# Performance work log

Hardware: AMD Instinct MI355X
Metric: run time of the kernel (lower is better)

The kernel has to match this reference:

```python
import jax, jax.numpy as jnp
import numpy as np

N = 50000      # nodes
E = 800000     # edges (before self loops)
G = 256        # graphs in batch
N_IN, NHID, HEADS, NOUT = 128, 64, 2, 768
ATT_SLOPE = 0.2   # GATv2 attention LeakyReLU slope (PyG default)
ACT_SLOPE = 0.01  # nn.LeakyReLU default slope


def setup_inputs() -> dict:
    key = jax.random.key(0)
    ks = jax.random.split(key, 20)
    def lin_w(k, fo, fi):
        return (jax.random.normal(k, (fo, fi), jnp.float32) / np.sqrt(fi)).astype(jnp.float32)
    x = jax.random.normal(ks[0], (N, N_IN), jnp.float32)
    edge_index = jax.random.randint(ks[1], (2, E), 0, N, dtype=jnp.int64)
    batch = jnp.sort(jax.random.randint(ks[2], (N,), 0, G, dtype=jnp.int64))
    HC = HEADS * NHID
    return {
        "x": x, "edge_index": edge_index, "batch": batch,
        # conv1: GATv2Conv(N_IN -> NHID, heads=HEADS)
        "w1_l": lin_w(ks[3], HC, N_IN), "b1_l": jnp.zeros((HC,), jnp.float32),
        "w1_r": lin_w(ks[4], HC, N_IN), "b1_r": jnp.zeros((HC,), jnp.float32),
        "att1": jax.random.normal(ks[5], (HEADS, NHID), jnp.float32) / np.sqrt(NHID),
        "bias1": jnp.zeros((HC,), jnp.float32),
        # conv2: GATv2Conv(HC -> NHID, heads=1)
        "w2_l": lin_w(ks[6], NHID, HC), "b2_l": jnp.zeros((NHID,), jnp.float32),
        "w2_r": lin_w(ks[7], NHID, HC), "b2_r": jnp.zeros((NHID,), jnp.float32),
        "att2": jax.random.normal(ks[8], (1, NHID), jnp.float32) / np.sqrt(NHID),
        "bias2": jnp.zeros((NHID,), jnp.float32),
        # MLP head
        "fc1_w": lin_w(ks[9], NHID, NHID), "fc1_b": jnp.zeros((NHID,), jnp.float32),
        "fc2_w": lin_w(ks[10], NOUT, NHID), "fc2_b": jnp.zeros((NOUT,), jnp.float32),
    }


def _leaky(v, slope):
    return jnp.where(v > 0, v, slope * v)


def gatv2_conv(x, src, dst, w_l, b_l, w_r, b_r, att, bias, heads, ch):
    n = x.shape[0]
    xl = (x @ w_l.T + b_l).reshape(n, heads, ch)   # source transform
    xr = (x @ w_r.T + b_r).reshape(n, heads, ch)   # target transform
    m = _leaky(xl[src] + xr[dst], ATT_SLOPE)       # [E, H, C]
    e = jnp.einsum('ehc,hc->eh', m, att)           # attention logits
    # segment softmax over incoming edges of each dst node (self loops guarantee non-empty)
    emax = jax.ops.segment_max(e, dst, num_segments=n)
    ex = jnp.exp(e - emax[dst])
    denom = jax.ops.segment_sum(ex, dst, num_segments=n)
    alpha = ex / denom[dst]
    out = jax.ops.segment_sum(xl[src] * alpha[:, :, None], dst, num_segments=n)
    return out.reshape(n, heads * ch) + bias


def reference(x, edge_index, batch, w1_l, b1_l, w1_r, b1_r, att1, bias1,
              w2_l, b2_l, w2_r, b2_r, att2, bias2, fc1_w, fc1_b, fc2_w, fc2_b):
    loops = jnp.arange(N, dtype=edge_index.dtype)
    src = jnp.concatenate([edge_index[0], loops])  # PyG adds self loops by default
    dst = jnp.concatenate([edge_index[1], loops])
    h = gatv2_conv(x, src, dst, w1_l, b1_l, w1_r, b1_r, att1, bias1, HEADS, NHID)
    h = _leaky(h, ACT_SLOPE)
    h = gatv2_conv(h, src, dst, w2_l, b2_l, w2_r, b2_r, att2, bias2, 1, NHID)
    h = _leaky(h, ACT_SLOPE)
    # global mean pool over graphs
    sums = jax.ops.segment_sum(h, batch, num_segments=G)
    cnt = jax.ops.segment_sum(jnp.ones((N,), h.dtype), batch, num_segments=G)
    pooled = sums / jnp.maximum(cnt, 1.0)[:, None]
    h = _leaky(pooled @ fc1_w.T + fc1_b, ACT_SLOPE)
    return h @ fc2_w.T + fc2_b
```

## Files before the change

### kernel.cpp

```cpp
#include <hip/hip_runtime.h>

#define ATT_SLOPE 0.2f
#define ACT_SLOPE 0.01f

typedef _Float16 half8  __attribute__((ext_vector_type(8)));
typedef _Float16 half2v __attribute__((ext_vector_type(2)));
typedef float    floatx4 __attribute__((ext_vector_type(4)));

#if defined(__has_builtin)
#if __has_builtin(__builtin_amdgcn_fdot2)
#define HAVE_FDOT2 1
#endif
#endif

__device__ __forceinline__ float lrelu(float v, float s) {
    return fmaxf(v, v * s);
}

__device__ __forceinline__ half2v lrelu2(half2v m) {
    half2v t = m * (_Float16)ATT_SLOPE;
    return __builtin_elementwise_max(m, t);
}

__device__ __forceinline__ float dot2(half2v a, half2v b, float c) {
#ifdef HAVE_FDOT2
    return __builtin_amdgcn_fdot2(a, b, c, false);
#else
    return c + (float)a[0] * (float)b[0] + (float)a[1] * (float)b[1];
#endif
}


__global__ __launch_bounds__(256) void k_count_rank(const int* __restrict__ ei, int E, int N,
                                                    int* __restrict__ deg,
                                                    int* __restrict__ rank) {
    int i = blockIdx.x * 256 + threadIdx.x;
    int total = E + N;
    if (i >= total) return;
    int dst = (i < E) ? ei[E + i] : (i - E);
    rank[i] = atomicAdd(&deg[dst], 1);
}

__global__ __launch_bounds__(256) void k_scan_block(const int* __restrict__ deg, int n,
                                                    int* __restrict__ rp1, int* __restrict__ bsum) {
    __shared__ int s[256];
    int tid = threadIdx.x;
    int i = blockIdx.x * 256 + tid;
    s[tid] = (i < n) ? deg[i] : 0;
    __syncthreads();
    for (int off = 1; off < 256; off <<= 1) {
        int t = (tid >= off) ? s[tid - off] : 0;
        __syncthreads();
        s[tid] += t;
        __syncthreads();
    }
    if (i < n) rp1[i] = s[tid];
    if (tid == 255) bsum[blockIdx.x] = s[255];
}

__global__ __launch_bounds__(256) void k_scan_add(int* __restrict__ rowptr,
                                                  const int* __restrict__ bsum, int n) {
    __shared__ int s[256];
    int tid = threadIdx.x, bid = blockIdx.x;
    s[tid] = (tid < bid) ? bsum[tid] : 0;
    __syncthreads();
    for (int off = 128; off > 0; off >>= 1) {
        if (tid < off) s[tid] += s[tid + off];
        __syncthreads();
    }
    int boff = s[0];
    int i = bid * 256 + tid;
    if (i < n) rowptr[i + 1] += boff;
    if (i == 0) rowptr[0] = 0;
}


__global__ __launch_bounds__(256) void k_encode_w(const float* __restrict__ w1l,
                                                  const float* __restrict__ w1r,
                                                  const float* __restrict__ w2l,
                                                  const float* __restrict__ w2r,
                                                  _Float16* __restrict__ W1h,
                                                  _Float16* __restrict__ W1lo,
                                                  _Float16* __restrict__ W2h,
                                                  _Float16* __restrict__ W2lo,
                                                  float* __restrict__ gsum, int gn,
                                                  int* __restrict__ deg, int n) {
    int i = blockIdx.x * 256 + threadIdx.x;
    if (i >= 49152 + gn + n) return;
    if (i >= 49152 + gn) {
        deg[i - 49152 - gn] = 0;
        return;
    }
    if (i >= 49152) {
        gsum[i - 49152] = 0.f;
        return;
    }
    float v;
    _Float16 *ph, *pl;
    int idx;
    if (i < 32768) {
        idx = i;
        v = (i < 16384) ? w1l[i] : w1r[i - 16384];
        ph = W1h; pl = W1lo;
    } else {
        int j = i - 32768;
        idx = j;
        v = (j < 8192) ? w2l[j] : w2r[j - 8192];
        ph = W2h; pl = W2lo;
    }
    _Float16 h = (_Float16)v;
    ph[idx] = h;
    pl[idx] = (_Float16)(v - (float)h);
}


template <int COUT, bool IN_F32>
__device__ __forceinline__ void gemm_body(int bid, int tid,
                                          _Float16 (*sWh)[40], _Float16 (*sWl)[40],
                                          const float* __restrict__ Af,
                                          const _Float16* __restrict__ Ahi,
                                          const _Float16* __restrict__ Alo, int n_rows,
                                          const _Float16* __restrict__ Whi,
                                          const _Float16* __restrict__ Wlo,
                                          const float* __restrict__ B0,
                                          const float* __restrict__ B1,
                                          _Float16* __restrict__ out) {
    constexpr int NT = COUT / 16;
    const int lane = tid & 63, wv = tid >> 6;
    const int m = lane & 15, q = lane >> 4;
    const long row0 = ((long)bid * 4 + wv) * 16;
    const bool active = row0 < n_rows;
    const long arow = row0 + m;

    floatx4 acc[NT] = {};
    for (int kk = 0; kk < 128; kk += 32) {
        __syncthreads();
        for (int t = tid; t < COUT * 4; t += 256) {
            int c = t >> 2, ch = t & 3;
            *(half8*)&sWh[c][ch * 8] = *(const half8*)&Whi[(size_t)c * 128 + kk + ch * 8];
            *(half8*)&sWl[c][ch * 8] = *(const half8*)&Wlo[(size_t)c * 128 + kk + ch * 8];
        }
        __syncthreads();
        if (active) {
            half8 ah, al;
            if constexpr (IN_F32) {
                float4 a0 = *(const float4*)&Af[(size_t)arow * 128 + kk + q * 8];
                float4 a1 = *(const float4*)&Af[(size_t)arow * 128 + kk + q * 8 + 4];
                float av[8] = {a0.x, a0.y, a0.z, a0.w, a1.x, a1.y, a1.z, a1.w};
                #pragma unroll
                for (int x = 0; x < 8; ++x) {
                    ah[x] = (_Float16)av[x];
                    al[x] = (_Float16)(av[x] - (float)ah[x]);
                }
            } else {
                ah = *(const half8*)&Ahi[(size_t)arow * 128 + kk + q * 8];
                al = *(const half8*)&Alo[(size_t)arow * 128 + kk + q * 8];
            }
            #pragma unroll
            for (int nt = 0; nt < NT; ++nt) {
                half8 bh = *(const half8*)&sWh[nt * 16 + m][q * 8];
                half8 bl = *(const half8*)&sWl[nt * 16 + m][q * 8];
                acc[nt] = __builtin_amdgcn_mfma_f32_16x16x32_f16(ah, bh, acc[nt], 0, 0, 0);
                acc[nt] = __builtin_amdgcn_mfma_f32_16x16x32_f16(al, bh, acc[nt], 0, 0, 0);
                acc[nt] = __builtin_amdgcn_mfma_f32_16x16x32_f16(ah, bl, acc[nt], 0, 0, 0);
            }
        }
    }
    if (active) {
        #pragma unroll
        for (int nt = 0; nt < NT; ++nt) {
            int col = nt * 16 + m;
            float b = (col < COUT / 2) ? B0[col] : B1[col - COUT / 2];
            #pragma unroll
            for (int r = 0; r < 4; ++r) {
                long grow = row0 + q * 4 + r;
                out[(size_t)grow * COUT + col] = (_Float16)(acc[nt][r] + b);
            }
        }
    }
}

__global__ __launch_bounds__(256) void k_gemm1_scatter(const float* __restrict__ x,
                                                       const _Float16* __restrict__ W1h,
                                                       const _Float16* __restrict__ W1lo,
                                                       const float* __restrict__ B0,
                                                       const float* __restrict__ B1,
                                                       _Float16* __restrict__ buf1, int n_rows,
                                                       const int* __restrict__ ei, int E,
                                                       const int* __restrict__ rowptr,
                                                       const int* __restrict__ rank,
                                                       int* __restrict__ adj, int gB) {
    __shared__ _Float16 sWh[256][40];
    __shared__ _Float16 sWl[256][40];
    const int bid = blockIdx.x, tid = threadIdx.x;
    if (bid < gB) {
        gemm_body<256, true>(bid, tid, sWh, sWl, x, nullptr, nullptr, n_rows,
                             W1h, W1lo, B0, B1, buf1);
    } else {
        int i = (bid - gB) * 256 + tid;
        int T = E + n_rows;
        if (i < T) {
            int dst = (i < E) ? ei[E + i] : (i - E);
            int src = (i < E) ? ei[i] : dst;
            adj[rowptr[dst] + rank[i]] = src;
        }
    }
}

template <int COUT, bool IN_F32>
__global__ __launch_bounds__(256) void gemm_mfma(const float* __restrict__ Af,
                                                 const _Float16* __restrict__ Ahi,
                                                 const _Float16* __restrict__ Alo, int n_rows,
                                                 const _Float16* __restrict__ Whi,
                                                 const _Float16* __restrict__ Wlo,
                                                 const float* __restrict__ B0,
                                                 const float* __restrict__ B1,
                                                 _Float16* __restrict__ out) {
    __shared__ _Float16 sWh[COUT][40];
    __shared__ _Float16 sWl[COUT][40];
    gemm_body<COUT, IN_F32>(blockIdx.x, threadIdx.x, sWh, sWl, Af, Ahi, Alo, n_rows,
                            Whi, Wlo, B0, B1, out);
}


__global__ __launch_bounds__(128) void conv1_fused(const _Float16* __restrict__ buf,
                                                   const int* __restrict__ rowptr,
                                                   const int* __restrict__ adj,
                                                   const float* __restrict__ att,
                                                   const float* __restrict__ bias,
                                                   _Float16* __restrict__ h1hi,
                                                   _Float16* __restrict__ h1lo, int n) {
    __shared__ _Float16 sxl[2][16][136];
    __shared__ _Float16 sxr[2][128];
    __shared__ float    sw[2][2][16];
    __shared__ _Float16 satt[128];
    const int tid = threadIdx.x, lane = tid & 63, wv = tid >> 6;
    satt[tid] = (_Float16)att[tid];
    __syncthreads();
    int node = blockIdx.x * 2 + wv;
    if (node >= n) return;

    const int jlane = lane & 15;
    const int grp = lane >> 4;
    const int chq = grp * 32;
    const int head = grp >> 1;
    const int wselg = lane >> 5;
    if (lane < 16)
        *(half8*)&sxr[wv][lane * 8] = *(const half8*)&buf[(size_t)node * 256 + 128 + lane * 8];
    asm volatile("s_waitcnt lgkmcnt(0)" ::: "memory");

    const int s = rowptr[node], e = rowptr[node + 1];
    float2 accA = {0.f, 0.f}, accB = {0.f, 0.f};
    float denA = 0.f, denB = 0.f;
    for (int c0 = s; c0 < e; c0 += 16) {
        const int cnt = min(16, e - c0);
        float sacc0 = 0.f, sacc1 = 0.f;
        if (jlane < cnt) {
            int src = adj[c0 + jlane];
            const _Float16* xlp = &buf[(size_t)src * 256 + chq];
            #pragma unroll
            for (int k = 0; k < 4; ++k) {
                half8 l = *(const half8*)&xlp[k * 8];
                half8 r = *(const half8*)&sxr[wv][chq + k * 8];
                half8 a = *(const half8*)&satt[chq + k * 8];
                *(half8*)&sxl[wv][jlane][chq + k * 8] = l;
                float* sp = (k & 1) ? &sacc1 : &sacc0;
                #pragma unroll
                for (int p = 0; p < 4; ++p) {
                    half2v lp = {l[2 * p], l[2 * p + 1]};
                    half2v rp = {r[2 * p], r[2 * p + 1]};
                    half2v ap = {a[2 * p], a[2 * p + 1]};
                    *sp = dot2(lrelu2(lp + rp), ap, *sp);
                }
            }
        }
        float sacc = sacc0 + sacc1;
        float efull = sacc + __shfl_xor(sacc, 16);
        if ((grp & 1) == 0 && jlane < cnt) sw[wv][head][jlane] = __expf(efull);
        asm volatile("s_waitcnt lgkmcnt(0)" ::: "memory");
        int j = 0;
        for (; j + 1 < cnt; j += 2) {
            float w0 = sw[wv][wselg][j], w1 = sw[wv][wselg][j + 1];
            half2v v0 = *(const half2v*)&sxl[wv][j][lane * 2];
            half2v v1 = *(const half2v*)&sxl[wv][j + 1][lane * 2];
            accA.x += w0 * (float)v0[0]; accA.y += w0 * (float)v0[1]; denA += w0;
            accB.x += w1 * (float)v1[0]; accB.y += w1 * (float)v1[1]; denB += w1;
        }
        if (j < cnt) {
            float w0 = sw[wv][wselg][j];
            half2v v0 = *(const half2v*)&sxl[wv][j][lane * 2];
            accA.x += w0 * (float)v0[0]; accA.y += w0 * (float)v0[1]; denA += w0;
        }
        asm volatile("s_waitcnt lgkmcnt(0)" ::: "memory");
    }
    float inv = 1.f / (denA + denB);
    float2 b = *(const float2*)&bias[lane * 2];
    float ox = lrelu((accA.x + accB.x) * inv + b.x, ACT_SLOPE);
    float oy = lrelu((accA.y + accB.y) * inv + b.y, ACT_SLOPE);
    half2v hv, lv;
    hv[0] = (_Float16)ox; lv[0] = (_Float16)(ox - (float)hv[0]);
    hv[1] = (_Float16)oy; lv[1] = (_Float16)(oy - (float)hv[1]);
    *(half2v*)&h1hi[(size_t)node * 128 + lane * 2] = hv;
    *(half2v*)&h1lo[(size_t)node * 128 + lane * 2] = lv;
}


__global__ __launch_bounds__(128) void conv2_fused(const _Float16* __restrict__ buf,
                                                   const int* __restrict__ rowptr,
                                                   const int* __restrict__ adj,
                                                   const float* __restrict__ att,
                                                   const float* __restrict__ bias,
                                                   const int* __restrict__ batch,
                                                   float* __restrict__ gsum, int n) {
    __shared__ _Float16 sxl[2][32][72];
    __shared__ _Float16 sxr[2][64];
    __shared__ float    sw[2][32];
    __shared__ _Float16 satt[64];
    const int tid = threadIdx.x, lane = tid & 63, wv = tid >> 6;
    if (tid < 64) satt[tid] = (_Float16)att[tid];
    __syncthreads();
    int node = blockIdx.x * 2 + wv;
    if (node >= n) return;

    const int j = lane & 31;
    const int g = lane >> 5;
    const int ch0 = g * 32;
    if (lane < 8)
        *(half8*)&sxr[wv][lane * 8] = *(const half8*)&buf[(size_t)node * 128 + 64 + lane * 8];
    asm volatile("s_waitcnt lgkmcnt(0)" ::: "memory");

    const int s = rowptr[node], e = rowptr[node + 1];
    float accA = 0.f, accB = 0.f, denA = 0.f, denB = 0.f;
    for (int c0 = s; c0 < e; c0 += 32) {
        const int cnt = min(32, e - c0);
        float sacc = 0.f;
        if (j < cnt) {
            int src = adj[c0 + j];
            const _Float16* xlp = &buf[(size_t)src * 128 + ch0];
            #pragma unroll
            for (int k = 0; k < 4; ++k) {
                half8 l = *(const half8*)&xlp[k * 8];
                half8 r = *(const half8*)&sxr[wv][ch0 + k * 8];
                half8 a = *(const half8*)&satt[ch0 + k * 8];
                *(half8*)&sxl[wv][j][ch0 + k * 8] = l;
                #pragma unroll
                for (int p = 0; p < 4; ++p) {
                    half2v lp = {l[2 * p], l[2 * p + 1]};
                    half2v rp = {r[2 * p], r[2 * p + 1]};
                    half2v ap = {a[2 * p], a[2 * p + 1]};
                    sacc = dot2(lrelu2(lp + rp), ap, sacc);
                }
            }
        }
        float efull = sacc + __shfl_xor(sacc, 32);
        if (g == 0 && j < cnt) sw[wv][j] = __expf(efull);
        asm volatile("s_waitcnt lgkmcnt(0)" ::: "memory");
        int jj = 0;
        for (; jj + 1 < cnt; jj += 2) {
            float w0 = sw[wv][jj], w1 = sw[wv][jj + 1];
            accA += w0 * (float)sxl[wv][jj][lane];     denA += w0;
            accB += w1 * (float)sxl[wv][jj + 1][lane]; denB += w1;
        }
        if (jj < cnt) {
            float w0 = sw[wv][jj];
            accA += w0 * (float)sxl[wv][jj][lane];
            denA += w0;
        }
        asm volatile("s_waitcnt lgkmcnt(0)" ::: "memory");
    }
    float val = lrelu((accA + accB) / (denA + denB) + bias[lane], ACT_SLOPE);
    atomicAdd(&gsum[(size_t)batch[node] * 64 + lane], val);
}


__device__ __forceinline__ int lower_bound(const int* a, int n, int v) {
    int lo = 0, hi = n;
    while (lo < hi) { int mid = (lo + hi) >> 1; if (a[mid] < v) lo = mid + 1; else hi = mid; }
    return lo;
}

__global__ __launch_bounds__(256) void pool_mlp(const float* __restrict__ gsum,
                                                const int* __restrict__ batch,
                                                const float* __restrict__ fc1_w,
                                                const float* __restrict__ fc1_b,
                                                const float* __restrict__ fc2_w,
                                                const float* __restrict__ fc2_b,
                                                float* __restrict__ out, int n) {
    const int g = blockIdx.x;
    const int tid = threadIdx.x;
    __shared__ float pooled[64];
    __shared__ float hmid[64];

    int lo = lower_bound(batch, n, g);
    int hi = lower_bound(batch, n, g + 1);
    float inv = 1.f / (float)max(hi - lo, 1);

    if (tid < 64) pooled[tid] = gsum[(size_t)g * 64 + tid] * inv;
    __syncthreads();
    if (tid < 64) {
        float acc = fc1_b[tid];
        const float* w = &fc1_w[(size_t)tid * 64];
        #pragma unroll
        for (int k = 0; k < 64; ++k) acc += pooled[k] * w[k];
        hmid[tid] = lrelu(acc, ACT_SLOPE);
    }
    __syncthreads();
    for (int o = tid; o < 768; o += 256) {
        float acc = fc2_b[o];
        const float* w = &fc2_w[(size_t)o * 64];
        #pragma unroll
        for (int k = 0; k < 64; ++k) acc += hmid[k] * w[k];
        out[(size_t)g * 768 + o] = acc;
    }
}


extern "C" void kernel_launch(void* const* d_in, const int* in_sizes, int n_in,
                              void* d_out, int out_size, void* d_ws, size_t ws_size,
                              hipStream_t stream) {
    const float* x     = (const float*)d_in[0];
    const int*   ei    = (const int*)d_in[1];
    const int*   batch = (const int*)d_in[2];
    const float* w1_l  = (const float*)d_in[3];
    const float* b1_l  = (const float*)d_in[4];
    const float* w1_r  = (const float*)d_in[5];
    const float* b1_r  = (const float*)d_in[6];
    const float* att1  = (const float*)d_in[7];
    const float* bias1 = (const float*)d_in[8];
    const float* w2_l  = (const float*)d_in[9];
    const float* b2_l  = (const float*)d_in[10];
    const float* w2_r  = (const float*)d_in[11];
    const float* b2_r  = (const float*)d_in[12];
    const float* att2  = (const float*)d_in[13];
    const float* bias2 = (const float*)d_in[14];
    const float* fc1_w = (const float*)d_in[15];
    const float* fc1_b = (const float*)d_in[16];
    const float* fc2_w = (const float*)d_in[17];
    const float* fc2_b = (const float*)d_in[18];
    float* out = (float*)d_out;

    const int N = in_sizes[2];
    const int E = in_sizes[1] / 2;
    const int T = E + N;
    const int G = out_size / 768;

    char* ws = (char*)d_ws;
    size_t off = 0;
    auto alloc = [&](size_t bytes) -> void* {
        void* p = ws + off;
        off = (off + bytes + 255) & ~(size_t)255;
        return p;
    };
    int*      deg    = (int*)alloc((size_t)N * 4);
    int*      rowptr = (int*)alloc((size_t)(N + 1) * 4);
    int*      rank   = (int*)alloc((size_t)T * 4);
    int*      bsum   = (int*)alloc(1024);
    int*      adj    = (int*)alloc((size_t)T * 4);
    _Float16* h1hi   = (_Float16*)alloc((size_t)N * 128 * 2);
    _Float16* h1lo   = (_Float16*)alloc((size_t)N * 128 * 2);
    _Float16* W1h    = (_Float16*)alloc(32768 * 2);
    _Float16* W1lo   = (_Float16*)alloc(32768 * 2);
    _Float16* W2h    = (_Float16*)alloc(16384 * 2);
    _Float16* W2lo   = (_Float16*)alloc(16384 * 2);
    float*    gsum   = (float*)alloc((size_t)G * 64 * 4);
    _Float16* buf1   = (_Float16*)alloc((size_t)N * 256 * 2);
    _Float16* buf2 = buf1;

    const int nbN  = (N + 255) / 256;
    const int nbT  = (T + 255) / 256;
    const int mfmG = (N / 16 + 3) / 4;
    const int edgG = (N + 1) / 2;
    const int encG = (49152 + G * 64 + N + 255) / 256;

    k_encode_w<<<encG, 256, 0, stream>>>(w1_l, w1_r, w2_l, w2_r,
                                         W1h, W1lo, W2h, W2lo, gsum, G * 64, deg, N);

    k_count_rank<<<nbT, 256, 0, stream>>>(ei, E, N, deg, rank);
    k_scan_block<<<nbN, 256, 0, stream>>>(deg, N, rowptr + 1, bsum);
    k_scan_add<<<nbN, 256, 0, stream>>>(rowptr, bsum, N);

    k_gemm1_scatter<<<mfmG + nbT, 256, 0, stream>>>(x, W1h, W1lo, b1_l, b1_r, buf1, N,
                                                    ei, E, rowptr, rank, adj, mfmG);

    conv1_fused<<<edgG, 128, 0, stream>>>(buf1, rowptr, adj, att1, bias1, h1hi, h1lo, N);

    gemm_mfma<128, false><<<mfmG, 256, 0, stream>>>(nullptr, h1hi, h1lo, N,
                                                    W2h, W2lo, b2_l, b2_r, buf2);
    conv2_fused<<<edgG, 128, 0, stream>>>(buf2, rowptr, adj, att2, bias2, batch, gsum, N);

    pool_mlp<<<G, 256, 0, stream>>>(gsum, batch, fc1_w, fc1_b, fc2_w, fc2_b, out, N);
}
```

Measured before the change: 298.0 us.

## Process nodes in descending-degree order via counting-sort permutation for load balance

Adds a degree histogram in the scan kernel and a new counting-sort kernel that builds a permutation of nodes ordered by descending in-degree (capped at 63). Both conv kernels now process nodes in that order, so high-degree nodes are scheduled first and similar-degree nodes share a block. This targets tail imbalance and divergence between the two waves of a block. It costs an extra kernel launch and an indirection. Output writes become scattered and lose coalescing, and the conv2 batch-pooling atomics lose their locality.

Measured after the change: 291.6 us, median of 2. -2.2%, faster.

```diff
diff --git a/kernel.cpp b/kernel.cpp
--- a/kernel.cpp
+++ b/kernel.cpp
@@ -42,12 +42,17 @@
 }
 
 __global__ __launch_bounds__(256) void k_scan_block(const int* __restrict__ deg, int n,
-                                                    int* __restrict__ rp1, int* __restrict__ bsum) {
+                                                    int* __restrict__ rp1, int* __restrict__ bsum,
+                                                    int* __restrict__ hist) {
     __shared__ int s[256];
+    __shared__ int lh[64];
     int tid = threadIdx.x;
     int i = blockIdx.x * 256 + tid;
-    s[tid] = (i < n) ? deg[i] : 0;
-    __syncthreads();
+    int dv = (i < n) ? deg[i] : 0;
+    s[tid] = dv;
+    if (tid < 64) lh[tid] = 0;
+    __syncthreads();
+    if (i < n) atomicAdd(&lh[min(dv, 63)], 1);
     for (int off = 1; off < 256; off <<= 1) {
         int t = (tid >= off) ? s[tid - off] : 0;
         __syncthreads();
@@ -56,6 +61,7 @@
     }
     if (i < n) rp1[i] = s[tid];
     if (tid == 255) bsum[blockIdx.x] = s[255];
+    if (tid < 64 && lh[tid]) atomicAdd(&hist[tid], lh[tid]);
 }
 
 __global__ __launch_bounds__(256) void k_scan_add(int* __restrict__ rowptr,
@@ -72,6 +78,27 @@
     int i = bid * 256 + tid;
     if (i < n) rowptr[i + 1] += boff;
     if (i == 0) rowptr[0] = 0;
+}
+
+__global__ __launch_bounds__(256) void k_perm(const int* __restrict__ deg, int n,
+                                              const int* __restrict__ hist,
+                                              int* __restrict__ cursor,
+                                              int* __restrict__ perm) {
+    __shared__ int lh[64], gb[64], bb[64];
+    int tid = threadIdx.x, i = blockIdx.x * 256 + tid;
+    if (tid < 64) lh[tid] = 0;
+    __syncthreads();
+    int b = 0, lpos = 0;
+    if (i < n) { b = min(deg[i], 63); lpos = atomicAdd(&lh[b], 1); }
+    __syncthreads();
+    if (tid < 64) {
+        gb[tid] = lh[tid] ? atomicAdd(&cursor[tid], lh[tid]) : 0;
+        int s = 0;
+        for (int k = 63; k > tid; --k) s += hist[k];
+        bb[tid] = s;
+    }
+    __syncthreads();
+    if (i < n) perm[bb[b] + gb[b] + lpos] = i;
 }
 
 
@@ -84,9 +111,14 @@
                                                   _Float16* __restrict__ W2h,
                                                   _Float16* __restrict__ W2lo,
                                                   float* __restrict__ gsum, int gn,
-                                                  int* __restrict__ deg, int n) {
+                                                  int* __restrict__ deg, int n,
+                                                  int* __restrict__ hc) {
     int i = blockIdx.x * 256 + threadIdx.x;
-    if (i >= 49152 + gn + n) return;
+    if (i >= 49152 + gn + n + 128) return;
+    if (i >= 49152 + gn + n) {
+        hc[i - 49152 - gn - n] = 0;
+        return;
+    }
     if (i >= 49152 + gn) {
         deg[i - 49152 - gn] = 0;
         return;
@@ -226,6 +258,7 @@
 __global__ __launch_bounds__(128) void conv1_fused(const _Float16* __restrict__ buf,
                                                    const int* __restrict__ rowptr,
                                                    const int* __restrict__ adj,
+                                                   const int* __restrict__ perm,
                                                    const float* __restrict__ att,
                                                    const float* __restrict__ bias,
                                                    _Float16* __restrict__ h1hi,
@@ -237,8 +270,9 @@
     const int tid = threadIdx.x, lane = tid & 63, wv = tid >> 6;
     satt[tid] = (_Float16)att[tid];
     __syncthreads();
-    int node = blockIdx.x * 2 + wv;
-    if (node >= n) return;
+    int idx = blockIdx.x * 2 + wv;
+    if (idx >= n) return;
+    int node = perm[idx];
 
     const int jlane = lane & 15;
     const int grp = lane >> 4;
@@ -308,6 +342,7 @@
 __global__ __launch_bounds__(128) void conv2_fused(const _Float16* __restrict__ buf,
                                                    const int* __restrict__ rowptr,
                                                    const int* __restrict__ adj,
+                                                   const int* __restrict__ perm,
                                                    const float* __restrict__ att,
                                                    const float* __restrict__ bias,
                                                    const int* __restrict__ batch,
@@ -319,8 +354,9 @@
     const int tid = threadIdx.x, lane = tid & 63, wv = tid >> 6;
     if (tid < 64) satt[tid] = (_Float16)att[tid];
     __syncthreads();
-    int node = blockIdx.x * 2 + wv;
-    if (node >= n) return;
+    int idx = blockIdx.x * 2 + wv;
+    if (idx >= n) return;
+    int node = perm[idx];
 
     const int j = lane & 31;
     const int g = lane >> 5;
@@ -455,6 +491,8 @@
     int*      rowptr = (int*)alloc((size_t)(N + 1) * 4);
     int*      rank   = (int*)alloc((size_t)T * 4);
     int*      bsum   = (int*)alloc(1024);
+    int*      hc     = (int*)alloc(128 * 4);
+    int*      perm   = (int*)alloc((size_t)N * 4);
     int*      adj    = (int*)alloc((size_t)T * 4);
     _Float16* h1hi   = (_Float16*)alloc((size_t)N * 128 * 2);
     _Float16* h1lo   = (_Float16*)alloc((size_t)N * 128 * 2);
@@ -465,28 +503,33 @@
     float*    gsum   = (float*)alloc((size_t)G * 64 * 4);
     _Float16* buf1   = (_Float16*)alloc((size_t)N * 256 * 2);
     _Float16* buf2 = buf1;
+    int* hist   = hc;
+    int* cursor = hc + 64;
 
     const int nbN  = (N + 255) / 256;
     const int nbT  = (T + 255) / 256;
     const int mfmG = (N / 16 + 3) / 4;
     const int edgG = (N + 1) / 2;
-    const int encG = (49152 + G * 64 + N + 255) / 256;
+    const int encG = (49152 + G * 64 + N + 128 + 255) / 256;
 
     k_encode_w<<<encG, 256, 0, stream>>>(w1_l, w1_r, w2_l, w2_r,
-                                         W1h, W1lo, W2h, W2lo, gsum, G * 64, deg, N);
+                                         W1h, W1lo, W2h, W2lo, gsum, G * 64, deg, N, hc);
 
     k_count_rank<<<nbT, 256, 0, stream>>>(ei, E, N, deg, rank);
-    k_scan_block<<<nbN, 256, 0, stream>>>(deg, N, rowptr + 1, bsum);
+    k_scan_block<<<nbN, 256, 0, stream>>>(deg, N, rowptr + 1, bsum, hist);
     k_scan_add<<<nbN, 256, 0, stream>>>(rowptr, bsum, N);
+    k_perm<<<nbN, 256, 0, stream>>>(deg, N, hist, cursor, perm);
 
     k_gemm1_scatter<<<mfmG + nbT, 256, 0, stream>>>(x, W1h, W1lo, b1_l, b1_r, buf1, N,
                                                     ei, E, rowptr, rank, adj, mfmG);
 
-    conv1_fused<<<edgG, 128, 0, stream>>>(buf1, rowptr, adj, att1, bias1, h1hi, h1lo, N);
+    conv1_fused<<<edgG, 128, 0, stream>>>(buf1, rowptr, adj, perm, att1, bias1,
+                                          h1hi, h1lo, N);
 
     gemm_mfma<128, false><<<mfmG, 256, 0, stream>>>(nullptr, h1hi, h1lo, N,
                                                     W2h, W2lo, b2_l, b2_r, buf2);
-    conv2_fused<<<edgG, 128, 0, stream>>>(buf2, rowptr, adj, att2, bias2, batch, gsum, N);
+    conv2_fused<<<edgG, 128, 0, stream>>>(buf2, rowptr, adj, perm, att2, bias2,
+                                          batch, gsum, N);
 
     pool_mlp<<<G, 256, 0, stream>>>(gsum, batch, fc1_w, fc1_b, fc2_w, fc2_b, out, N);
 }
```
